# Performance work log

Measured on AMD Instinct MI355X. Metric: run time of the kernel, lower is better.

Reference implementation:

```python
import jax, jax.numpy as jnp
import numpy as np

N = 100000          # num_nodes
E = 1250000         # num_edges
H = 64              # node_hidden_size
T = 2               # num_rounds


def setup_inputs() -> dict:
    key = jax.random.key(0)
    ks = jax.random.split(key, 10)
    s = 0.1  # init scale for weights
    return {
        "x": jax.random.normal(ks[0], (N, H), dtype=jnp.float32),
        "edge_index": jax.random.randint(ks[1], (2, E), 0, N, dtype=jnp.int64),
        "edge_attr": jax.random.normal(ks[2], (E, 1), dtype=jnp.float32),
        # message layers: Linear(2H+1 -> H), one per round
        "msg_W": jax.random.normal(ks[3], (T, H, 2 * H + 1), dtype=jnp.float32) * s,
        "msg_b": jax.random.normal(ks[4], (T, H), dtype=jnp.float32) * s,
        # GRUCell params, gate order (r, z, n) as in torch
        "gru_Wih": jax.random.normal(ks[5], (T, 3 * H, H), dtype=jnp.float32) * s,
        "gru_bih": jax.random.normal(ks[6], (T, 3 * H), dtype=jnp.float32) * s,
        "gru_Whh": jax.random.normal(ks[7], (T, 3 * H, H), dtype=jnp.float32) * s,
        "gru_bhh": jax.random.normal(ks[8], (T, 3 * H), dtype=jnp.float32) * s,
    }


def _gru_cell(inp, h, Wih, bih, Whh, bhh):
    # torch.nn.GRUCell math, gate order r, z, n
    gi = inp @ Wih.T + bih   # [N, 3H]
    gh = h @ Whh.T + bhh     # [N, 3H]
    i_r, i_z, i_n = jnp.split(gi, 3, axis=1)
    h_r, h_z, h_n = jnp.split(gh, 3, axis=1)
    r = jax.nn.sigmoid(i_r + h_r)
    z = jax.nn.sigmoid(i_z + h_z)
    n = jnp.tanh(i_n + r * h_n)
    return (1.0 - z) * n + z * h


def reference(x, edge_index, edge_attr, msg_W, msg_b, gru_Wih, gru_bih, gru_Whh, gru_bhh):
    row, col = edge_index[0], edge_index[1]
    num_rounds = msg_W.shape[0]
    for t in range(num_rounds):
        src = x[row]    # [E, H]
        dest = x[col]   # [E, H]
        m_input = jnp.concatenate([dest, src, edge_attr], axis=1)  # [E, 2H+1]
        messages = m_input @ msg_W[t].T + msg_b[t]                 # [E, H]
        agg = jax.ops.segment_sum(messages, row, num_segments=x.shape[0])  # [N, H]
        x = _gru_cell(agg, x, gru_Wih[t], gru_bih[t], gru_Whh[t], gru_bhh[t])
    return x
```

## Files before the change

### kernel.cpp

```cpp
#include <hip/hip_runtime.h>
#include <hip/hip_bf16.h>
#include <hip/hip_fp16.h>

#define H 64
#define CAP 48

typedef __attribute__((ext_vector_type(8))) short short8;
typedef __attribute__((ext_vector_type(4))) float float4v;

__device__ __forceinline__ short f2bf_bits(float f) {
    union { __hip_bfloat16 b; short s; } u;
    u.b = __float2bfloat16(f);
    return u.s;
}
__device__ __forceinline__ float bf2f(unsigned short s) {
    union { unsigned int u; float f; } v;
    v.u = ((unsigned int)s) << 16;
    return v.f;
}
__device__ __forceinline__ void split8(const float* p, short8& hi, short8& lo) {
    float4v f0 = *(const float4v*)p;
    float4v f1 = *(const float4v*)(p + 4);
#pragma unroll
    for (int j = 0; j < 8; j++) {
        float f = (j < 4) ? f0[j] : f1[j - 4];
        short h = f2bf_bits(f);
        float fh = bf2f((unsigned short)h);
        hi[j] = h;
        lo[j] = f2bf_bits(f - fh);
    }
}
__device__ __forceinline__ void zero8(short8& hi, short8& lo) {
#pragma unroll
    for (int j = 0; j < 8; j++) { hi[j] = 0; lo[j] = 0; }
}

#define MFMA(a, b, c) __builtin_amdgcn_mfma_f32_16x16x32_bf16(a, b, c, 0, 0, 0)

__global__ __launch_bounds__(256) void count_prep(
    const int* __restrict__ row, int* __restrict__ deg, int* __restrict__ lpos,
    int E, int EB,
    const float* __restrict__ msg_W,
    const float* __restrict__ Wih, const float* __restrict__ Whh,
    short* __restrict__ msgfrag, short* __restrict__ grufrag, int T)
{
    if ((int)blockIdx.x < EB) {
        int e = blockIdx.x * 256 + threadIdx.x;
        if (e < E) lpos[e] = atomicAdd(&deg[row[e]], 1);
        return;
    }
    const int lane = threadIdx.x & 63;
    int unit = (blockIdx.x - EB) * 4 + (threadIdx.x >> 6);
    const int kq = (lane >> 4) * 8;
    if (unit < T * 16) {
        const int slot = unit & 15, t = unit >> 4;
        const int tile = slot >> 1, ks = slot & 1;
        const float* W = msg_W + (size_t)t * H * 129;
        const int wrow = (tile & 3) * 16 + (lane & 15);
        const int coff = (tile < 4) ? 0 : 64;
        short8 hi, lo;
        split8(W + (size_t)wrow * 129 + coff + ks * 32 + kq, hi, lo);
        short8* out = (short8*)(msgfrag + (size_t)t * 16384);
        out[slot * 64 + lane] = hi;
        out[16 * 64 + slot * 64 + lane] = lo;
    } else {
        unit -= T * 16;
        if (unit >= T * 48) return;
        const int slot = unit % 48, t = unit / 48;
        const int tile = slot >> 1, ks = slot & 1;
        const float* Wp = (tile < 12)
            ? (Wih + (size_t)t * 192 * H + ((size_t)(tile * 16 + (lane & 15))) * H)
            : (Whh + (size_t)t * 192 * H + ((size_t)((tile - 12) * 16 + (lane & 15))) * H);
        short8 hi, lo;
        split8(Wp + ks * 32 + kq, hi, lo);
        short8* out = (short8*)(grufrag + (size_t)t * 49152);
        out[slot * 64 + lane] = hi;
        out[48 * 64 + slot * 64 + lane] = lo;
    }
}

__global__ __launch_bounds__(256) void scatter_cast(
    const int* __restrict__ row, const int* __restrict__ col,
    const float* __restrict__ attr, const int* __restrict__ lpos,
    int2* __restrict__ edata, int E, int EB,
    const float* __restrict__ x_in, __half* __restrict__ xh, int NH8)
{
    if ((int)blockIdx.x < EB) {
        int e = blockIdx.x * 256 + threadIdx.x;
        if (e < E) {
            int p = lpos[e];
            if (p < CAP) {
                int2 v;
                v.x = col[e];
                v.y = __float_as_int(attr[e]);
                edata[(size_t)row[e] * CAP + p] = v;
            }
        }
    } else {
        int i = (blockIdx.x - EB) * 256 + threadIdx.x;
        if (i < NH8) {
            const float* p = x_in + (size_t)i * 8;
            float4v f0 = *(const float4v*)p;
            float4v f1 = *(const float4v*)(p + 4);
            short8 hv;
#pragma unroll
            for (int u = 0; u < 8; u++) {
                float f = (u < 4) ? f0[u] : f1[u - 4];
                hv[u] = __half_as_short(__float2half(f));
            }
            *(short8*)(xh + (size_t)i * 8) = hv;
        }
    }
}

__global__ __launch_bounds__(64) void aggregate(
    const int* __restrict__ deg, const int2* __restrict__ edata,
    const __half* __restrict__ xh,
    short* __restrict__ s_hi, short* __restrict__ s_lo,
    float2* __restrict__ asum2, int N)
{
    const int lane = threadIdx.x & 63;
    const int g = lane >> 3, cl = lane & 7;
    const int n = blockIdx.x * 8 + g;
    int cnt = 0;
    if (n < N) { cnt = deg[n]; if (cnt > CAP) cnt = CAP; }
    const int2* ebase = edata + (size_t)n * CAP;
    float acc[8] = {0.f,0.f,0.f,0.f,0.f,0.f,0.f,0.f};
    float aacc = 0.f;
    for (int j = 0; j < cnt; j += 8) {
        int2 e[8];
#pragma unroll
        for (int u = 0; u < 8; u++) {
            int idx = j + u; if (idx > cnt - 1) idx = cnt - 1;
            e[u] = ebase[idx];
        }
        short8 h[8];
#pragma unroll
        for (int u = 0; u < 8; u++) {
            int c = e[u].x;
            c = (c < 0) ? 0 : (c >= N ? N - 1 : c);
            h[u] = *(const short8*)(xh + (size_t)c * H + cl * 8);
        }
#pragma unroll
        for (int u = 0; u < 8; u++) {
            const bool val = (j + u < cnt);
            const float w = val ? 1.f : 0.f;
            aacc += val ? __int_as_float(e[u].y) : 0.f;
#pragma unroll
            for (int k = 0; k < 8; k++)
                acc[k] = fmaf(w, __half2float(__ushort_as_half((unsigned short)h[u][k])), acc[k]);
        }
    }
    if (n < N) {
        short8 hi8, lo8;
#pragma unroll
        for (int u = 0; u < 8; u++) {
            float v = acc[u];
            short hbits = f2bf_bits(v);
            hi8[u] = hbits;
            lo8[u] = f2bf_bits(v - bf2f((unsigned short)hbits));
        }
        *(short8*)(s_hi + (size_t)n * H + cl * 8) = hi8;
        *(short8*)(s_lo + (size_t)n * H + cl * 8) = lo8;
        if (cl == 0) asum2[n] = make_float2(aacc, (float)cnt);
    }
}

#define SLD 68
__global__ __launch_bounds__(64) void fused_msg_gru(
    const short* __restrict__ s_hi, const short* __restrict__ s_lo,
    const float2* __restrict__ asum2,
    const float* xf,
    float* x, __half* __restrict__ xh,
    const short* __restrict__ mfrag, const short* __restrict__ gfrag,
    const float* __restrict__ Wt, const float* __restrict__ mb,
    const float* __restrict__ bih, const float* __restrict__ bhh,
    int N, int write_xh)
{
    __shared__ float scratch[16 * SLD];
    const int lane = threadIdx.x & 63;
    const int base = blockIdx.x * 16;
    if (base >= N) return;
    const int arow = lane & 15;
    const int kq = (lane >> 4) * 8;
    const int colb = lane & 15;
    const int rq4 = (lane >> 4) * 4;
    const int m_a = base + arow;
    const bool mv = (m_a < N);
    const short8* mhi = (const short8*)mfrag;
    const short8* mlo = mhi + 16 * 64;
    const short8* ghi = (const short8*)gfrag;
    const short8* glo = ghi + 48 * 64;
    float* scr = scratch;

    short8 sfh[2], sfl[2], xfh[2], xfl[2];
#pragma unroll
    for (int ks = 0; ks < 2; ks++) {
        if (mv) {
            sfh[ks] = *(const short8*)(s_hi + (size_t)m_a * H + ks * 32 + kq);
            sfl[ks] = *(const short8*)(s_lo + (size_t)m_a * H + ks * 32 + kq);
            split8(xf + (size_t)m_a * H + ks * 32 + kq, xfh[ks], xfl[ks]);
        } else { zero8(sfh[ks], sfl[ks]); zero8(xfh[ks], xfl[ks]); }
    }
    float2 da[4];
#pragma unroll
    for (int r = 0; r < 4; r++) {
        const int m = base + rq4 + r;
        da[r] = (m < N) ? asum2[m] : make_float2(0.f, 0.f);
    }

    float4v accd[4], accs[4];
#pragma unroll
    for (int ct = 0; ct < 4; ct++) {
        accd[ct] = (float4v){0.f, 0.f, 0.f, 0.f};
        accs[ct] = (float4v){0.f, 0.f, 0.f, 0.f};
    }
#pragma unroll
    for (int ks = 0; ks < 2; ks++) {
#pragma unroll
        for (int ct = 0; ct < 4; ct++) {
            short8 bh = mhi[(ct * 2 + ks) * 64 + lane];
            short8 bl = mlo[(ct * 2 + ks) * 64 + lane];
            accd[ct] = MFMA(sfh[ks], bh, accd[ct]);
            accd[ct] = MFMA(sfl[ks], bh, accd[ct]);
            accd[ct] = MFMA(sfh[ks], bl, accd[ct]);
            short8 ch = mhi[((4 + ct) * 2 + ks) * 64 + lane];
            short8 cl8 = mlo[((4 + ct) * 2 + ks) * 64 + lane];
            accs[ct] = MFMA(xfh[ks], ch, accs[ct]);
            accs[ct] = MFMA(xfl[ks], ch, accs[ct]);
            accs[ct] = MFMA(xfh[ks], cl8, accs[ct]);
        }
    }

#pragma unroll
    for (int ct = 0; ct < 4; ct++) {
        const int j = ct * 16 + colb;
        const float bj = mb[j];
        const float wa = Wt[(size_t)j * 129 + 128];
#pragma unroll
        for (int r = 0; r < 4; r++) {
            float v = accd[ct][r] + da[r].y * (accs[ct][r] + bj) + da[r].x * wa;
            scr[(rq4 + r) * SLD + j] = v;
        }
    }
    asm volatile("s_waitcnt lgkmcnt(0)" ::: "memory");
    short8 agh[2], agl[2];
#pragma unroll
    for (int ks = 0; ks < 2; ks++)
        split8(scr + arow * SLD + ks * 32 + kq, agh[ks], agl[ks]);

#pragma unroll
    for (int ct = 0; ct < 4; ct++) {
        float4v ai[3], ao[3];
#pragma unroll
        for (int g2 = 0; g2 < 3; g2++) {
            ai[g2] = (float4v){0.f, 0.f, 0.f, 0.f};
            ao[g2] = (float4v){0.f, 0.f, 0.f, 0.f};
        }
#pragma unroll
        for (int ks = 0; ks < 2; ks++) {
#pragma unroll
            for (int g2 = 0; g2 < 3; g2++) {
                short8 bh = ghi[((g2 * 4 + ct) * 2 + ks) * 64 + lane];
                short8 bl = glo[((g2 * 4 + ct) * 2 + ks) * 64 + lane];
                ai[g2] = MFMA(agh[ks], bh, ai[g2]);
                ai[g2] = MFMA(agl[ks], bh, ai[g2]);
                ai[g2] = MFMA(agh[ks], bl, ai[g2]);
                short8 hh = ghi[((12 + g2 * 4 + ct) * 2 + ks) * 64 + lane];
                short8 hl = glo[((12 + g2 * 4 + ct) * 2 + ks) * 64 + lane];
                ao[g2] = MFMA(xfh[ks], hh, ao[g2]);
                ao[g2] = MFMA(xfl[ks], hh, ao[g2]);
                ao[g2] = MFMA(xfh[ks], hl, ao[g2]);
            }
        }
        const int j = ct * 16 + colb;
        const float b_ir = bih[j], b_iz = bih[64 + j], b_in = bih[128 + j];
        const float b_hr = bhh[j], b_hz = bhh[64 + j], b_hn = bhh[128 + j];
#pragma unroll
        for (int r = 0; r < 4; r++) {
            const int m = base + rq4 + r;
            float ir = ai[0][r] + b_ir;
            float iz = ai[1][r] + b_iz;
            float in_ = ai[2][r] + b_in;
            float hr = ao[0][r] + b_hr;
            float hz = ao[1][r] + b_hz;
            float hn = ao[2][r] + b_hn;
            float rr = 1.f / (1.f + __expf(-(ir + hr)));
            float zz = 1.f / (1.f + __expf(-(iz + hz)));
            float e2 = __expf(2.f * (in_ + rr * hn));
            float nn = 1.f - 2.f / (e2 + 1.f);
            float hold = (m < N) ? xf[(size_t)m * H + j] : 0.f;
            scr[(rq4 + r) * SLD + j] = (1.f - zz) * nn + zz * hold;
        }
    }
    asm volatile("s_waitcnt lgkmcnt(0)" ::: "memory");

    if (mv) {
        float4v o[4];
#pragma unroll
        for (int q4 = 0; q4 < 4; q4++)
            o[q4] = *(const float4v*)(scr + arow * SLD + (lane >> 4) * 16 + q4 * 4);
        float4v* xp = (float4v*)(x + (size_t)m_a * H + (lane >> 4) * 16);
        xp[0] = o[0]; xp[1] = o[1]; xp[2] = o[2]; xp[3] = o[3];
        if (write_xh) {
            short8 hv0, hv1;
#pragma unroll
            for (int u = 0; u < 8; u++) {
                hv0[u] = __half_as_short(__float2half(o[u >> 2][u & 3]));
                hv1[u] = __half_as_short(__float2half(o[2 + (u >> 2)][u & 3]));
            }
            *(short8*)(xh + (size_t)m_a * H + (lane >> 4) * 16) = hv0;
            *(short8*)(xh + (size_t)m_a * H + (lane >> 4) * 16 + 8) = hv1;
        }
    }
}

extern "C" void kernel_launch(void* const* d_in, const int* in_sizes, int n_in,
                              void* d_out, int out_size, void* d_ws, size_t ws_size,
                              hipStream_t stream) {
    const float* x_in  = (const float*)d_in[0];
    const int*   ei    = (const int*)d_in[1];
    const float* attr  = (const float*)d_in[2];
    const float* msg_W = (const float*)d_in[3];
    const float* msg_b = (const float*)d_in[4];
    const float* Wih   = (const float*)d_in[5];
    const float* bih   = (const float*)d_in[6];
    const float* Whh   = (const float*)d_in[7];
    const float* bhh   = (const float*)d_in[8];

    const int N = in_sizes[0] / H;
    const int E = in_sizes[2];
    const int T = in_sizes[4] / H;
    const int* row = ei;
    const int* col = ei + E;

    float*  x       = (float*)d_out;
    short*  s_hi    = (short*)d_ws;
    short*  s_lo    = s_hi + (size_t)N * H;
    int*    lpos    = (int*)s_lo;
    __half* xh      = (__half*)(s_lo + (size_t)N * H);
    float2* asum2   = (float2*)(xh + (size_t)N * H);
    int*    deg     = (int*)(asum2 + N);
    int2*   edata   = (int2*)(deg + N);
    short*  msgfrag = (short*)(edata + (size_t)N * CAP);
    short*  grufrag = msgfrag + (size_t)T * 16384;

    const int eb  = (E + 255) / 256;
    const int nh8 = (N * H) / 8;
    const int cb  = (nh8 + 255) / 256;
    const int pb  = (T * 16 + T * 48 + 3) / 4;

    hipMemsetAsync(deg, 0, (size_t)N * sizeof(int), stream);

    count_prep<<<eb + pb, 256, 0, stream>>>(
        row, deg, lpos, E, eb, msg_W, Wih, Whh, msgfrag, grufrag, T);
    scatter_cast<<<eb + cb, 256, 0, stream>>>(
        row, col, attr, lpos, edata, E, eb, x_in, xh, nh8);

    const int agg_blocks = (N + 7) / 8;
    const int fus_blocks = (N + 15) / 16;

    for (int t = 0; t < T; t++) {
        aggregate<<<agg_blocks, 64, 0, stream>>>(
            deg, edata, xh, s_hi, s_lo, asum2, N);
        fused_msg_gru<<<fus_blocks, 64, 0, stream>>>(
            s_hi, s_lo, asum2,
            (t == 0) ? x_in : x, x, xh,
            msgfrag + (size_t)t * 16384, grufrag + (size_t)t * 49152,
            msg_W + (size_t)t * H * (2 * H + 1), msg_b + (size_t)t * H,
            bih + (size_t)t * 3 * H, bhh + (size_t)t * 3 * H,
            N, (t + 1 < T) ? 1 : 0);
    }
}
```

Baseline: 335.3 us.

## Fuse neighbor aggregation into message+GRU kernel with ping-pong half buffers

Merges the gather-sum aggregation kernel into the fused message/GRU kernel. Each 16-node block now aggregates its own rows into shared memory instead of writing split bf16 hi/lo sums and degree data to global memory and reading them back. Because other blocks still read the half-precision node features while this block writes updated ones, the fp16 copy is double-buffered across rounds. This removes one launch per round and the global round-trip of the aggregate, at the cost of more serial work per block and fewer co-resident independent waves to hide gather latency.

```diff
diff --git a/kernel.cpp b/kernel.cpp
--- a/kernel.cpp
+++ b/kernel.cpp
@@ -113,71 +113,19 @@
     }
 }
 
-__global__ __launch_bounds__(64) void aggregate(
+#define SLD 68
+__global__ __launch_bounds__(64) void agg_msg_gru(
     const int* __restrict__ deg, const int2* __restrict__ edata,
-    const __half* __restrict__ xh,
-    short* __restrict__ s_hi, short* __restrict__ s_lo,
-    float2* __restrict__ asum2, int N)
-{
-    const int lane = threadIdx.x & 63;
-    const int g = lane >> 3, cl = lane & 7;
-    const int n = blockIdx.x * 8 + g;
-    int cnt = 0;
-    if (n < N) { cnt = deg[n]; if (cnt > CAP) cnt = CAP; }
-    const int2* ebase = edata + (size_t)n * CAP;
-    float acc[8] = {0.f,0.f,0.f,0.f,0.f,0.f,0.f,0.f};
-    float aacc = 0.f;
-    for (int j = 0; j < cnt; j += 8) {
-        int2 e[8];
-#pragma unroll
-        for (int u = 0; u < 8; u++) {
-            int idx = j + u; if (idx > cnt - 1) idx = cnt - 1;
-            e[u] = ebase[idx];
-        }
-        short8 h[8];
-#pragma unroll
-        for (int u = 0; u < 8; u++) {
-            int c = e[u].x;
-            c = (c < 0) ? 0 : (c >= N ? N - 1 : c);
-            h[u] = *(const short8*)(xh + (size_t)c * H + cl * 8);
-        }
-#pragma unroll
-        for (int u = 0; u < 8; u++) {
-            const bool val = (j + u < cnt);
-            const float w = val ? 1.f : 0.f;
-            aacc += val ? __int_as_float(e[u].y) : 0.f;
-#pragma unroll
-            for (int k = 0; k < 8; k++)
-                acc[k] = fmaf(w, __half2float(__ushort_as_half((unsigned short)h[u][k])), acc[k]);
-        }
-    }
-    if (n < N) {
-        short8 hi8, lo8;
-#pragma unroll
-        for (int u = 0; u < 8; u++) {
-            float v = acc[u];
-            short hbits = f2bf_bits(v);
-            hi8[u] = hbits;
-            lo8[u] = f2bf_bits(v - bf2f((unsigned short)hbits));
-        }
-        *(short8*)(s_hi + (size_t)n * H + cl * 8) = hi8;
-        *(short8*)(s_lo + (size_t)n * H + cl * 8) = lo8;
-        if (cl == 0) asum2[n] = make_float2(aacc, (float)cnt);
-    }
-}
-
-#define SLD 68
-__global__ __launch_bounds__(64) void fused_msg_gru(
-    const short* __restrict__ s_hi, const short* __restrict__ s_lo,
-    const float2* __restrict__ asum2,
+    const __half* __restrict__ xh_r,
     const float* xf,
-    float* x, __half* __restrict__ xh,
+    float* x, __half* __restrict__ xh_w,
     const short* __restrict__ mfrag, const short* __restrict__ gfrag,
     const float* __restrict__ Wt, const float* __restrict__ mb,
     const float* __restrict__ bih, const float* __restrict__ bhh,
     int N, int write_xh)
 {
     __shared__ float scratch[16 * SLD];
+    __shared__ float2 adeg[16];
     const int lane = threadIdx.x & 63;
     const int base = blockIdx.x * 16;
     if (base >= N) return;
@@ -185,69 +133,96 @@
     const int kq = (lane >> 4) * 8;
     const int colb = lane & 15;
     const int rq4 = (lane >> 4) * 4;
-    const int m_a = base + arow;
-    const bool mv = (m_a < N);
+    const int g = lane >> 3, cl = lane & 7;
     const short8* mhi = (const short8*)mfrag;
     const short8* mlo = mhi + 16 * 64;
     const short8* ghi = (const short8*)gfrag;
     const short8* glo = ghi + 48 * 64;
-    float* scr = scratch;
-
+
+#pragma unroll
+    for (int p = 0; p < 2; p++) {
+        const int n = base + p * 8 + g;
+        int cnt = 0;
+        if (n < N) { cnt = deg[n]; if (cnt > CAP) cnt = CAP; }
+        const int2* ebase = edata + (size_t)n * CAP;
+        float acc[8] = {0.f,0.f,0.f,0.f,0.f,0.f,0.f,0.f};
+        float aacc = 0.f;
+        for (int j = 0; j < cnt; j += 8) {
+            int2 e[8];
+#pragma unroll
+            for (int u = 0; u < 8; u++) {
+                int idx = j + u; if (idx > cnt - 1) idx = cnt - 1;
+                e[u] = ebase[idx];
+            }
+            short8 h[8];
+#pragma unroll
+            for (int u = 0; u < 8; u++) {
+                int c = e[u].x;
+                c = (c < 0) ? 0 : (c >= N ? N - 1 : c);
+                h[u] = *(const short8*)(xh_r + (size_t)c * H + cl * 8);
+            }
+#pragma unroll
+            for (int u = 0; u < 8; u++) {
+                const bool val = (j + u < cnt);
+                const float w = val ? 1.f : 0.f;
+                aacc += val ? __int_as_float(e[u].y) : 0.f;
+#pragma unroll
+                for (int k = 0; k < 8; k++)
+                    acc[k] = fmaf(w, __half2float(__ushort_as_half((unsigned short)h[u][k])), acc[k]);
+            }
+        }
+        float* sr = scratch + (p * 8 + g) * SLD + cl * 8;
+        *(float4v*)sr       = (float4v){acc[0], acc[1], acc[2], acc[3]};
+        *(float4v*)(sr + 4) = (float4v){acc[4], acc[5], acc[6], acc[7]};
+        if (cl == 0) adeg[p * 8 + g] = make_float2(aacc, (float)cnt);
+    }
+    asm volatile("s_waitcnt lgkmcnt(0)" ::: "memory");
+
+    float2 da[4];
+#pragma unroll
+    for (int r = 0; r < 4; r++) da[r] = adeg[rq4 + r];
+
+    const int m_a = base + arow;
+    const bool mv = (m_a < N);
     short8 sfh[2], sfl[2], xfh[2], xfl[2];
 #pragma unroll
     for (int ks = 0; ks < 2; ks++) {
-        if (mv) {
-            sfh[ks] = *(const short8*)(s_hi + (size_t)m_a * H + ks * 32 + kq);
-            sfl[ks] = *(const short8*)(s_lo + (size_t)m_a * H + ks * 32 + kq);
-            split8(xf + (size_t)m_a * H + ks * 32 + kq, xfh[ks], xfl[ks]);
-        } else { zero8(sfh[ks], sfl[ks]); zero8(xfh[ks], xfl[ks]); }
-    }
-    float2 da[4];
-#pragma unroll
-    for (int r = 0; r < 4; r++) {
-        const int m = base + rq4 + r;
-        da[r] = (m < N) ? asum2[m] : make_float2(0.f, 0.f);
-    }
-
-    float4v accd[4], accs[4];
+        split8(scratch + arow * SLD + ks * 32 + kq, sfh[ks], sfl[ks]);
+        if (mv) split8(xf + (size_t)m_a * H + ks * 32 + kq, xfh[ks], xfl[ks]);
+        else    zero8(xfh[ks], xfl[ks]);
+    }
+
 #pragma unroll
     for (int ct = 0; ct < 4; ct++) {
-        accd[ct] = (float4v){0.f, 0.f, 0.f, 0.f};
-        accs[ct] = (float4v){0.f, 0.f, 0.f, 0.f};
-    }
-#pragma unroll
-    for (int ks = 0; ks < 2; ks++) {
-#pragma unroll
-        for (int ct = 0; ct < 4; ct++) {
+        float4v accd = (float4v){0.f, 0.f, 0.f, 0.f};
+        float4v accs = (float4v){0.f, 0.f, 0.f, 0.f};
+#pragma unroll
+        for (int ks = 0; ks < 2; ks++) {
             short8 bh = mhi[(ct * 2 + ks) * 64 + lane];
             short8 bl = mlo[(ct * 2 + ks) * 64 + lane];
-            accd[ct] = MFMA(sfh[ks], bh, accd[ct]);
-            accd[ct] = MFMA(sfl[ks], bh, accd[ct]);
-            accd[ct] = MFMA(sfh[ks], bl, accd[ct]);
             short8 ch = mhi[((4 + ct) * 2 + ks) * 64 + lane];
             short8 cl8 = mlo[((4 + ct) * 2 + ks) * 64 + lane];
-            accs[ct] = MFMA(xfh[ks], ch, accs[ct]);
-            accs[ct] = MFMA(xfl[ks], ch, accs[ct]);
-            accs[ct] = MFMA(xfh[ks], cl8, accs[ct]);
-        }
-    }
-
-#pragma unroll
-    for (int ct = 0; ct < 4; ct++) {
+            accd = MFMA(sfh[ks], bh, accd);
+            accd = MFMA(sfl[ks], bh, accd);
+            accd = MFMA(sfh[ks], bl, accd);
+            accs = MFMA(xfh[ks], ch, accs);
+            accs = MFMA(xfl[ks], ch, accs);
+            accs = MFMA(xfh[ks], cl8, accs);
+        }
         const int j = ct * 16 + colb;
         const float bj = mb[j];
         const float wa = Wt[(size_t)j * 129 + 128];
 #pragma unroll
         for (int r = 0; r < 4; r++) {
-            float v = accd[ct][r] + da[r].y * (accs[ct][r] + bj) + da[r].x * wa;
-            scr[(rq4 + r) * SLD + j] = v;
+            float v = accd[r] + da[r].y * (accs[r] + bj) + da[r].x * wa;
+            scratch[(rq4 + r) * SLD + j] = v;
         }
     }
     asm volatile("s_waitcnt lgkmcnt(0)" ::: "memory");
     short8 agh[2], agl[2];
 #pragma unroll
     for (int ks = 0; ks < 2; ks++)
-        split8(scr + arow * SLD + ks * 32 + kq, agh[ks], agl[ks]);
+        split8(scratch + arow * SLD + ks * 32 + kq, agh[ks], agl[ks]);
 
 #pragma unroll
     for (int ct = 0; ct < 4; ct++) {
@@ -263,11 +238,11 @@
             for (int g2 = 0; g2 < 3; g2++) {
                 short8 bh = ghi[((g2 * 4 + ct) * 2 + ks) * 64 + lane];
                 short8 bl = glo[((g2 * 4 + ct) * 2 + ks) * 64 + lane];
+                short8 hh = ghi[((12 + g2 * 4 + ct) * 2 + ks) * 64 + lane];
+                short8 hl = glo[((12 + g2 * 4 + ct) * 2 + ks) * 64 + lane];
                 ai[g2] = MFMA(agh[ks], bh, ai[g2]);
                 ai[g2] = MFMA(agl[ks], bh, ai[g2]);
                 ai[g2] = MFMA(agh[ks], bl, ai[g2]);
-                short8 hh = ghi[((12 + g2 * 4 + ct) * 2 + ks) * 64 + lane];
-                short8 hl = glo[((12 + g2 * 4 + ct) * 2 + ks) * 64 + lane];
                 ao[g2] = MFMA(xfh[ks], hh, ao[g2]);
                 ao[g2] = MFMA(xfl[ks], hh, ao[g2]);
                 ao[g2] = MFMA(xfh[ks], hl, ao[g2]);
@@ -290,7 +265,7 @@
             float e2 = __expf(2.f * (in_ + rr * hn));
             float nn = 1.f - 2.f / (e2 + 1.f);
             float hold = (m < N) ? xf[(size_t)m * H + j] : 0.f;
-            scr[(rq4 + r) * SLD + j] = (1.f - zz) * nn + zz * hold;
+            scratch[(rq4 + r) * SLD + j] = (1.f - zz) * nn + zz * hold;
         }
     }
     asm volatile("s_waitcnt lgkmcnt(0)" ::: "memory");
@@ -299,7 +274,7 @@
         float4v o[4];
 #pragma unroll
         for (int q4 = 0; q4 < 4; q4++)
-            o[q4] = *(const float4v*)(scr + arow * SLD + (lane >> 4) * 16 + q4 * 4);
+            o[q4] = *(const float4v*)(scratch + arow * SLD + (lane >> 4) * 16 + q4 * 4);
         float4v* xp = (float4v*)(x + (size_t)m_a * H + (lane >> 4) * 16);
         xp[0] = o[0]; xp[1] = o[1]; xp[2] = o[2]; xp[3] = o[3];
         if (write_xh) {
@@ -309,8 +284,8 @@
                 hv0[u] = __half_as_short(__float2half(o[u >> 2][u & 3]));
                 hv1[u] = __half_as_short(__float2half(o[2 + (u >> 2)][u & 3]));
             }
-            *(short8*)(xh + (size_t)m_a * H + (lane >> 4) * 16) = hv0;
-            *(short8*)(xh + (size_t)m_a * H + (lane >> 4) * 16 + 8) = hv1;
+            *(short8*)(xh_w + (size_t)m_a * H + (lane >> 4) * 16) = hv0;
+            *(short8*)(xh_w + (size_t)m_a * H + (lane >> 4) * 16 + 8) = hv1;
         }
     }
 }
@@ -335,12 +310,10 @@
     const int* col = ei + E;
 
     float*  x       = (float*)d_out;
-    short*  s_hi    = (short*)d_ws;
-    short*  s_lo    = s_hi + (size_t)N * H;
-    int*    lpos    = (int*)s_lo;
-    __half* xh      = (__half*)(s_lo + (size_t)N * H);
-    float2* asum2   = (float2*)(xh + (size_t)N * H);
-    int*    deg     = (int*)(asum2 + N);
+    __half* xh_a    = (__half*)d_ws;
+    __half* xh_b    = xh_a + (size_t)N * H;
+    int*    lpos    = (int*)(xh_b + (size_t)N * H);
+    int*    deg     = lpos + E;
     int2*   edata   = (int2*)(deg + N);
     short*  msgfrag = (short*)(edata + (size_t)N * CAP);
     short*  grufrag = msgfrag + (size_t)T * 16384;
@@ -355,17 +328,16 @@
     count_prep<<<eb + pb, 256, 0, stream>>>(
         row, deg, lpos, E, eb, msg_W, Wih, Whh, msgfrag, grufrag, T);
     scatter_cast<<<eb + cb, 256, 0, stream>>>(
-        row, col, attr, lpos, edata, E, eb, x_in, xh, nh8);
-
-    const int agg_blocks = (N + 7) / 8;
-    const int fus_blocks = (N + 15) / 16;
+        row, col, attr, lpos, edata, E, eb, x_in, xh_a, nh8);
+
+    const int mg_blocks = (N + 15) / 16;
 
     for (int t = 0; t < T; t++) {
-        aggregate<<<agg_blocks, 64, 0, stream>>>(
-            deg, edata, xh, s_hi, s_lo, asum2, N);
-        fused_msg_gru<<<fus_blocks, 64, 0, stream>>>(
-            s_hi, s_lo, asum2,
-            (t == 0) ? x_in : x, x, xh,
+        const __half* xh_r = (t & 1) ? xh_b : xh_a;
+        __half*       xh_w = (t & 1) ? xh_a : xh_b;
+        agg_msg_gru<<<mg_blocks, 64, 0, stream>>>(
+            deg, edata, xh_r,
+            (t == 0) ? x_in : x, x, xh_w,
             msgfrag + (size_t)t * 16384, grufrag + (size_t)t * 49152,
             msg_W + (size_t)t * H * (2 * H + 1), msg_b + (size_t)t * H,
             bih + (size_t)t * 3 * H, bhh + (size_t)t * 3 * H,
```

After: 318.5 us (median of 2 runs). 1.05x faster.
